# Performance work log

Hardware: AMD Instinct MI355X
Metric: run time of the kernel (lower is better)

## Reference

```python
import jax, jax.numpy as jnp
import numpy as np

B, F_CH, K, N = 8, 512, 8, 2048

def sl3_basis():
    # Chevalley-style basis of sl(3,R): 2 diagonal (traceless) + 6 off-diagonal generators
    E = np.zeros((8, 3, 3), np.float32)
    E[0] = [[1, 0, 0], [0, -1, 0], [0, 0, 0]]
    E[1] = [[0, 1, 0], [0, 0, 0], [0, 0, 0]]
    E[2] = [[0, 0, 1], [0, 0, 0], [0, 0, 0]]
    E[3] = [[0, 0, 0], [1, 0, 0], [0, 0, 0]]
    E[4] = [[0, 0, 0], [0, 1, 0], [0, 0, -1]]
    E[5] = [[0, 0, 0], [0, 0, 1], [0, 0, 0]]
    E[6] = [[0, 0, 0], [0, 0, 0], [1, 0, 0]]
    E[7] = [[0, 0, 0], [0, 0, 0], [0, 1, 0]]
    return jnp.asarray(E)

def setup_inputs() -> dict:
    key = jax.random.key(0)
    kx, kw = jax.random.split(key)
    x = jax.random.normal(kx, (B, F_CH, K, N), dtype=jnp.float32)
    # learn_dir = nn.Linear(F, F, bias=False); weight is [out, in]
    W = jax.random.normal(kw, (F_CH, F_CH), dtype=jnp.float32) * (1.0 / np.sqrt(F_CH))
    return {"x": x, "W": W}

def reference(x, W):
    # x: [B, F, 8, N]; W: [F, F]
    E = sl3_basis()                                   # [8, 3, 3]
    # Killing form of sl(3): K(X, Y) = 6 * tr(X Y). Since hat() is linear in v,
    # K(hat(a), hat(b)) = a^T G b with Gram matrix G_ab = 6 * tr(E_a E_b).
    G = 6.0 * jnp.einsum('aij,bji->ab', E, E)         # [8, 8]
    # learn_dir applied over channel axis F (equivalent to transpose(1,-1) + Linear)
    d = jnp.einsum('bfkn,gf->bgkn', x, W)             # [B, F, 8, N]
    # killing form of x_hat with d_hat, per (b, f, n)
    kf = jnp.einsum('bfkn,kl,bfln->bfn', x, G, d)[:, :, None, :]  # [B, F, 1, N]
    # torch.where(kf <= 0, x, x - -kf * d)  ==  x + kf * d on the positive branch
    return jnp.where(kf <= 0, x, x + kf * d)
```

## Files before the change

### kernel.cpp

```cpp
#include <hip/hip_runtime.h>


typedef short bf16x8 __attribute__((ext_vector_type(8)));
typedef short bf16x4 __attribute__((ext_vector_type(4)));
typedef float f32x4 __attribute__((ext_vector_type(4)));

__device__ __forceinline__ unsigned short f2bf(float f) {
  unsigned int u = __float_as_uint(f);
  u += 0x7fffu + ((u >> 16) & 1u);
  return (unsigned short)(u >> 16);
}

__device__ __forceinline__ float bfu(unsigned short u) {
  return __uint_as_float(((unsigned int)u) << 16);
}

__global__ __launch_bounds__(256) void prepack_w(const float* __restrict__ W,
                                                 short* __restrict__ wp) {
  const int cid = blockIdx.x * 256 + threadIdx.x;
  const int row  = cid & 511;
  const int kgkt = cid >> 9;
  const int kg = kgkt & 3;
  const int kt = kgkt >> 2;
  const float* src = W + (size_t)row * 512 + kt * 32 + kg * 8;
  bf16x8 v;
#pragma unroll
  for (int j = 0; j < 8; ++j) v[j] = (short)f2bf(src[j]);
  *(bf16x8*)&wp[(size_t)cid * 8] = v;
}

__global__ __launch_bounds__(1024, 4) void lnkill_fullg4(
    const float* __restrict__ x, const short* __restrict__ wp,
    float* __restrict__ out) {
  __shared__ __align__(16) short ldsX[16][4096];

  const int tid   = threadIdx.x;
  const int lane  = tid & 63;
  const int w     = tid >> 6;
  const int klane = lane >> 4;
  const int li    = lane & 15;

  const int bid = blockIdx.x;
  const int nt  = bid & 127;
  const int b   = bid >> 7;
  const int n0  = nt * 16;

  const int kgs = tid >> 8;
  const int cm  = (tid >> 1) & 127;
  const int j0  = (tid & 1) * 4;
  const float* xs = x + (((size_t)(b * 512 + kgs * 8 + j0)) * 8 + (cm >> 4)) * 2048
                      + n0 + (cm & 15);
  const int bwr = tid * 4;

  f32x4 acc[2][8] = {};
  float rB[2][4];

  {
    float b0[4];
#pragma unroll
    for (int jj = 0; jj < 4; ++jj) b0[jj] = xs[(size_t)jj * 16384];
#pragma unroll
    for (int jj = 0; jj < 4; ++jj) rB[1][jj] = xs[(size_t)(32 + jj) * 16384];
    bf16x4 v;
#pragma unroll
    for (int jj = 0; jj < 4; ++jj) v[jj] = (short)f2bf(b0[jj]);
    *(bf16x4*)&ldsX[0][bwr] = v;
  }
  __syncthreads();

#pragma unroll
  for (int kt = 0; kt < 16; ++kt) {
    if (kt < 15) {
      bf16x4 v;
#pragma unroll
      for (int jj = 0; jj < 4; ++jj) v[jj] = (short)f2bf(rB[(kt + 1) & 1][jj]);
      *(bf16x4*)&ldsX[kt + 1][bwr] = v;
    }
    if (kt < 14) {
#pragma unroll
      for (int jj = 0; jj < 4; ++jj)
        rB[kt & 1][jj] = xs[(size_t)((kt + 2) * 32 + jj) * 16384];
    }

    const short* wt = wp + ((size_t)(kt * 4 + klane) * 512 + w * 32 + li) * 8;
    bf16x8 afr0 = *(const bf16x8*)(wt);
    bf16x8 afr1 = *(const bf16x8*)(wt + 128);
    const short* Bc = ldsX[kt];
    bf16x8 bfr[8];
#pragma unroll
    for (int fn = 0; fn < 8; ++fn)
      bfr[fn] = *(const bf16x8*)&Bc[(klane * 128 + fn * 16 + li) * 8];
#pragma unroll
    for (int fn = 0; fn < 8; ++fn)
      acc[0][fn] = __builtin_amdgcn_mfma_f32_16x16x32_bf16(afr0, bfr[fn],
                                                           acc[0][fn], 0, 0, 0);
#pragma unroll
    for (int fn = 0; fn < 8; ++fn)
      acc[1][fn] = __builtin_amdgcn_mfma_f32_16x16x32_bf16(afr1, bfr[fn],
                                                           acc[1][fn], 0, 0, 0);

    if (kt < 15) __syncthreads();
  }

  const unsigned short* xls = (const unsigned short*)&ldsX[w][0];
#pragma unroll
  for (int fm = 0; fm < 2; ++fm) {
#pragma unroll
    for (int r = 0; r < 4; ++r) {
      const int g = w * 32 + fm * 16 + klane * 4 + r;
      const size_t base = ((size_t)(b * 512 + g)) * 16384 + n0 + li;
      const int kgd = fm * 2 + (klane >> 1);
      const int jd  = (klane & 1) * 4 + r;
      float xk[8];
#pragma unroll
      for (int k = 0; k < 8; ++k)
        xk[k] = bfu(xls[(kgd * 128 + k * 16 + li) * 8 + jd]);
      const float c0 = 12.f * xk[0] - 6.f * xk[4];
      const float c4 = 12.f * xk[4] - 6.f * xk[0];
      const float c1 = 6.f * xk[3];
      const float c2 = 6.f * xk[6];
      const float c3 = 6.f * xk[1];
      const float c5 = 6.f * xk[7];
      const float c6 = 6.f * xk[2];
      const float c7 = 6.f * xk[5];
      const float kf = c0 * acc[fm][0][r] + c1 * acc[fm][1][r]
                     + c2 * acc[fm][2][r] + c3 * acc[fm][3][r]
                     + c4 * acc[fm][4][r] + c5 * acc[fm][5][r]
                     + c6 * acc[fm][6][r] + c7 * acc[fm][7][r];
#pragma unroll
      for (int k = 0; k < 8; ++k) {
        const float o = (kf <= 0.f) ? xk[k] : fmaf(kf, acc[fm][k][r], xk[k]);
        out[base + (size_t)k * 2048] = o;
      }
    }
  }
}

__global__ __launch_bounds__(512, 4) void lnkill_fused(
    const float* __restrict__ x, const float* __restrict__ W,
    float* __restrict__ out) {
  __shared__ __align__(16) short ldsA[2][4096];
  __shared__ __align__(16) short ldsB[2][4096];

  const int tid  = threadIdx.x;
  const int lane = tid & 63;
  const int w    = tid >> 6;

  const int bid = blockIdx.x;
  const int l   = (bid & 7) * 512 + (bid >> 3);
  const int gt  = l & 3;
  const int nt  = (l >> 2) & 127;
  const int b   = l >> 9;
  const int g0  = gt * 128;
  const int n0  = nt * 16;

  const int cm = tid & 127;
  const int fg = tid >> 7;
  const float* xs   = x + (((size_t)(b * 512 + fg * 8)) * 8 + (cm >> 4)) * 2048
                        + n0 + (cm & 15);
  const float* Wrow = W + (size_t)(g0 + cm) * 512 + fg * 8;

  f32x4 acc[8] = {};

  {
    float xv[8];
#pragma unroll
    for (int j = 0; j < 8; ++j) xv[j] = xs[(size_t)j * 16384];
    float4 wv[2];
    const float4* wpp = (const float4*)Wrow;
    wv[0] = wpp[0]; wv[1] = wpp[1];
    const float* wf = (const float*)wv;
    bf16x8 vb, va;
#pragma unroll
    for (int j = 0; j < 8; ++j) {
      vb[j] = (short)f2bf(xv[j]);
      va[j] = (short)f2bf(wf[j]);
    }
    *(bf16x8*)&ldsB[0][(fg * 128 + cm) * 8] = vb;
    *(bf16x8*)&ldsA[0][(fg * 128 + cm) * 8] = va;
  }
  __syncthreads();

  const int klane = lane >> 4;
  const int li    = lane & 15;

  for (int kt = 0; kt < 16; ++kt) {
    const int cur = kt & 1;
    float xv[8];
    float4 wv[2];
    if (kt < 15) {
      const float* xpn = xs + (size_t)(kt + 1) * 32 * 16384;
#pragma unroll
      for (int j = 0; j < 8; ++j) xv[j] = xpn[(size_t)j * 16384];
      const float4* wpp = (const float4*)(Wrow + (kt + 1) * 32);
      wv[0] = wpp[0]; wv[1] = wpp[1];
    }
    {
      const short* Ac = ldsA[cur];
      const short* Bc = ldsB[cur];
      bf16x8 afr = *(const bf16x8*)&Ac[(klane * 128 + w * 16 + li) * 8];
#pragma unroll
      for (int fn = 0; fn < 8; ++fn) {
        bf16x8 bfr = *(const bf16x8*)&Bc[(klane * 128 + fn * 16 + li) * 8];
        acc[fn] = __builtin_amdgcn_mfma_f32_16x16x32_bf16(afr, bfr, acc[fn], 0, 0, 0);
      }
    }
    if (kt < 15) {
      const int nxt = cur ^ 1;
      const float* wf = (const float*)wv;
      bf16x8 vb, va;
#pragma unroll
      for (int j = 0; j < 8; ++j) {
        vb[j] = (short)f2bf(xv[j]);
        va[j] = (short)f2bf(wf[j]);
      }
      __syncthreads();
      *(bf16x8*)&ldsB[nxt][(fg * 128 + cm) * 8] = vb;
      *(bf16x8*)&ldsA[nxt][(fg * 128 + cm) * 8] = va;
      __syncthreads();
    }
  }

#pragma unroll
  for (int r = 0; r < 4; ++r) {
    const int g = g0 + w * 16 + klane * 4 + r;
    const size_t base = ((size_t)(b * 512 + g)) * 16384 + n0 + li;
    float xk[8];
#pragma unroll
    for (int k = 0; k < 8; ++k) xk[k] = x[base + (size_t)k * 2048];
    const float c0 = 12.f * xk[0] - 6.f * xk[4];
    const float c4 = 12.f * xk[4] - 6.f * xk[0];
    const float c1 = 6.f * xk[3];
    const float c2 = 6.f * xk[6];
    const float c3 = 6.f * xk[1];
    const float c5 = 6.f * xk[7];
    const float c6 = 6.f * xk[2];
    const float c7 = 6.f * xk[5];
    const float kf = c0 * acc[0][r] + c1 * acc[1][r]
                   + c2 * acc[2][r] + c3 * acc[3][r]
                   + c4 * acc[4][r] + c5 * acc[5][r]
                   + c6 * acc[6][r] + c7 * acc[7][r];
#pragma unroll
    for (int k = 0; k < 8; ++k) {
      const float o = (kf <= 0.f) ? xk[k] : fmaf(kf, acc[k][r], xk[k]);
      out[base + (size_t)k * 2048] = o;
    }
  }
}

extern "C" void kernel_launch(void* const* d_in, const int* in_sizes, int n_in,
                              void* d_out, int out_size, void* d_ws, size_t ws_size,
                              hipStream_t stream) {
  const float* x = (const float*)d_in[0];
  const float* W = (const float*)d_in[1];
  float* out = (float*)d_out;

  if (ws_size >= (size_t)524288) {
    short* wp = (short*)d_ws;
    prepack_w<<<dim3(128), dim3(256), 0, stream>>>(W, wp);
    lnkill_fullg4<<<dim3(1024), dim3(1024), 0, stream>>>(x, wp, out);
  } else {
    lnkill_fused<<<dim3(4096), dim3(512), 0, stream>>>(x, W, out);
  }
}
```

Baseline: 182.2 us.

## Stage x into LDS in two halves to cut per-step barriers

The K loop used to run 16 steps with a __syncthreads after each one. It now converts and stores the first 8 K-tiles of x into LDS before a single barrier. The first 8 MFMA steps are computed while the remaining 8 tiles are written, then one more barrier precedes the last 8 steps, so there are only two barriers instead of sixteen. The B-fragment loads are also interleaved with the MFMAs instead of all being loaded up front. In exchange, the prologue becomes longer and its loads are less overlapped with compute.

```diff
diff --git a/kernel.cpp b/kernel.cpp
--- a/kernel.cpp
+++ b/kernel.cpp
@@ -29,7 +29,7 @@
   *(bf16x8*)&wp[(size_t)cid * 8] = v;
 }
 
-__global__ __launch_bounds__(1024, 4) void lnkill_fullg4(
+__global__ __launch_bounds__(1024, 4) void lnkill_fullg6(
     const float* __restrict__ x, const short* __restrict__ wp,
     float* __restrict__ out) {
   __shared__ __align__(16) short ldsX[16][4096];
@@ -55,51 +55,64 @@
   f32x4 acc[2][8] = {};
   float rB[2][4];
 
-  {
-    float b0[4];
-#pragma unroll
-    for (int jj = 0; jj < 4; ++jj) b0[jj] = xs[(size_t)jj * 16384];
-#pragma unroll
-    for (int jj = 0; jj < 4; ++jj) rB[1][jj] = xs[(size_t)(32 + jj) * 16384];
+#pragma unroll
+  for (int jj = 0; jj < 4; ++jj) rB[0][jj] = xs[(size_t)jj * 16384];
+#pragma unroll
+  for (int jj = 0; jj < 4; ++jj) rB[1][jj] = xs[(size_t)(32 + jj) * 16384];
+#pragma unroll
+  for (int t = 0; t < 8; ++t) {
     bf16x4 v;
 #pragma unroll
-    for (int jj = 0; jj < 4; ++jj) v[jj] = (short)f2bf(b0[jj]);
-    *(bf16x4*)&ldsX[0][bwr] = v;
+    for (int jj = 0; jj < 4; ++jj) v[jj] = (short)f2bf(rB[t & 1][jj]);
+    *(bf16x4*)&ldsX[t][bwr] = v;
+#pragma unroll
+    for (int jj = 0; jj < 4; ++jj)
+      rB[t & 1][jj] = xs[(size_t)((t + 2) * 32 + jj) * 16384];
   }
   __syncthreads();
 
 #pragma unroll
-  for (int kt = 0; kt < 16; ++kt) {
-    if (kt < 15) {
+  for (int kt = 0; kt < 8; ++kt) {
+    {
       bf16x4 v;
 #pragma unroll
-      for (int jj = 0; jj < 4; ++jj) v[jj] = (short)f2bf(rB[(kt + 1) & 1][jj]);
-      *(bf16x4*)&ldsX[kt + 1][bwr] = v;
-    }
-    if (kt < 14) {
+      for (int jj = 0; jj < 4; ++jj) v[jj] = (short)f2bf(rB[kt & 1][jj]);
+      *(bf16x4*)&ldsX[kt + 8][bwr] = v;
+    }
+    if (kt < 6) {
 #pragma unroll
       for (int jj = 0; jj < 4; ++jj)
-        rB[kt & 1][jj] = xs[(size_t)((kt + 2) * 32 + jj) * 16384];
-    }
-
+        rB[kt & 1][jj] = xs[(size_t)((kt + 10) * 32 + jj) * 16384];
+    }
     const short* wt = wp + ((size_t)(kt * 4 + klane) * 512 + w * 32 + li) * 8;
     bf16x8 afr0 = *(const bf16x8*)(wt);
     bf16x8 afr1 = *(const bf16x8*)(wt + 128);
     const short* Bc = ldsX[kt];
-    bf16x8 bfr[8];
-#pragma unroll
-    for (int fn = 0; fn < 8; ++fn)
-      bfr[fn] = *(const bf16x8*)&Bc[(klane * 128 + fn * 16 + li) * 8];
-#pragma unroll
-    for (int fn = 0; fn < 8; ++fn)
-      acc[0][fn] = __builtin_amdgcn_mfma_f32_16x16x32_bf16(afr0, bfr[fn],
+#pragma unroll
+    for (int fn = 0; fn < 8; ++fn) {
+      bf16x8 bfr = *(const bf16x8*)&Bc[(klane * 128 + fn * 16 + li) * 8];
+      acc[0][fn] = __builtin_amdgcn_mfma_f32_16x16x32_bf16(afr0, bfr,
                                                            acc[0][fn], 0, 0, 0);
-#pragma unroll
-    for (int fn = 0; fn < 8; ++fn)
-      acc[1][fn] = __builtin_amdgcn_mfma_f32_16x16x32_bf16(afr1, bfr[fn],
+      acc[1][fn] = __builtin_amdgcn_mfma_f32_16x16x32_bf16(afr1, bfr,
                                                            acc[1][fn], 0, 0, 0);
-
-    if (kt < 15) __syncthreads();
+    }
+  }
+  __syncthreads();
+
+#pragma unroll
+  for (int kt = 8; kt < 16; ++kt) {
+    const short* wt = wp + ((size_t)(kt * 4 + klane) * 512 + w * 32 + li) * 8;
+    bf16x8 afr0 = *(const bf16x8*)(wt);
+    bf16x8 afr1 = *(const bf16x8*)(wt + 128);
+    const short* Bc = ldsX[kt];
+#pragma unroll
+    for (int fn = 0; fn < 8; ++fn) {
+      bf16x8 bfr = *(const bf16x8*)&Bc[(klane * 128 + fn * 16 + li) * 8];
+      acc[0][fn] = __builtin_amdgcn_mfma_f32_16x16x32_bf16(afr0, bfr,
+                                                           acc[0][fn], 0, 0, 0);
+      acc[1][fn] = __builtin_amdgcn_mfma_f32_16x16x32_bf16(afr1, bfr,
+                                                           acc[1][fn], 0, 0, 0);
+    }
   }
 
   const unsigned short* xls = (const unsigned short*)&ldsX[w][0];
@@ -258,7 +271,7 @@
   if (ws_size >= (size_t)524288) {
     short* wp = (short*)d_ws;
     prepack_w<<<dim3(128), dim3(256), 0, stream>>>(W, wp);
-    lnkill_fullg4<<<dim3(1024), dim3(1024), 0, stream>>>(x, wp, out);
+    lnkill_fullg6<<<dim3(1024), dim3(1024), 0, stream>>>(x, wp, out);
   } else {
     lnkill_fused<<<dim3(4096), dim3(512), 0, stream>>>(x, W, out);
   }
```

After: 175.2 us (median of 2 runs). -3.8%, faster.
